# Performance work log

Hardware: AMD Instinct MI355X
Metric: run time of the kernel (lower is better)

Reference implementation:

```python
import jax, jax.numpy as jnp
import numpy as np

B, S, D, H = 2, 2048, 1024, 16
DK = D // H


def setup_inputs() -> dict:
    key = jax.random.key(0)
    ks = jax.random.split(key, 11)
    std = 1.0 / np.sqrt(D)
    return {
        "q": jax.random.normal(ks[0], (B, S, D), jnp.float32),
        "k": jax.random.normal(ks[1], (B, S, D), jnp.float32),
        "v": jax.random.normal(ks[2], (B, S, D), jnp.float32),
        "wq": jax.random.uniform(ks[3], (D, D), jnp.float32, -std, std),
        "bq": jax.random.uniform(ks[4], (D,), jnp.float32, -std, std),
        "wk": jax.random.uniform(ks[5], (D, D), jnp.float32, -std, std),
        "bk": jax.random.uniform(ks[6], (D,), jnp.float32, -std, std),
        "wv": jax.random.uniform(ks[7], (D, D), jnp.float32, -std, std),
        "bv": jax.random.uniform(ks[8], (D,), jnp.float32, -std, std),
        "wo": jax.random.uniform(ks[9], (D, D), jnp.float32, -std, std),
        "bo": jax.random.uniform(ks[10], (D,), jnp.float32, -std, std),
    }


def reference(q, k, v, wq, bq, wk, bk, wv, bv, wo, bo):
    b = q.shape[0]
    # QKV projections (nn.Linear: x @ W.T + b), split into heads -> [b, h, s, dk]
    def proj(x, w, bias):
        y = x @ w.T + bias
        return y.reshape(b, -1, H, DK).transpose(0, 2, 1, 3)

    qh, kh, vh = proj(q, wq, bq), proj(k, wk, bk), proj(v, wv, bv)
    scale = 1.0 / jnp.sqrt(jnp.float32(DK))
    scores = jnp.einsum("bhqd,bhkd->bhqk", qh, kh) * scale  # [b,h,s,s]
    attn = jax.nn.softmax(scores, axis=-1)
    out = jnp.einsum("bhqk,bhkd->bhqd", attn, vh)
    out = out.transpose(0, 2, 1, 3).reshape(b, -1, D)
    out = out @ wo.T + bo
    return out, attn
```

## Files before the change

kernel.cpp:

```cpp
#include <hip/hip_runtime.h>
#include <stdint.h>

#define H 16
#define SEQ 2048
#define DMODEL 1024
#define DK 64

typedef __attribute__((ext_vector_type(8))) short bf16x8;
typedef __attribute__((ext_vector_type(4))) float f32x4;
typedef __attribute__((ext_vector_type(4))) short s16x4;

__device__ __forceinline__ short f2bf(float f) {
  unsigned u = __float_as_uint(f);
  u += 0x7fffu + ((u >> 16) & 1u);
  return (short)(u >> 16);
}

__device__ __forceinline__ f32x4 mfma16(bf16x8 a, bf16x8 b, f32x4 c) {
  return __builtin_amdgcn_mfma_f32_16x16x32_bf16(a, b, c, 0, 0, 0);
}

__global__ void cast_bf16_kernel(const float* __restrict__ src,
                                 short* __restrict__ dst, int n4) {
  int i = blockIdx.x * blockDim.x + threadIdx.x;
  if (i < n4) {
    const float4 v = ((const float4*)src)[i];
    s16x4 o;
    o[0] = f2bf(v.x); o[1] = f2bf(v.y); o[2] = f2bf(v.z); o[3] = f2bf(v.w);
    ((s16x4*)dst)[i] = o;
  }
}

template <int EPI>
__global__ __launch_bounds__(256, 2) void gemm_nt(const short* __restrict__ A,
                                                  const short* __restrict__ Bm,
                                                  const float* __restrict__ bias,
                                                  void* __restrict__ outp) {
  __shared__ short Asub[128 * 32];
  __shared__ short Bsub[128 * 32];
  const int tid = threadIdx.x;
  const int lane = tid & 63, wid = tid >> 6;
  const int g = lane >> 4, ln = lane & 15;
  const int wr = wid >> 1, wc = wid & 1;
  const int m0 = blockIdx.y * 128, n0 = blockIdx.x * 128;

  f32x4 acc[4][4] = {};
  const int f0 = tid, f1 = tid + 256;

  for (int kt = 0; kt < 32; ++kt) {
    const int k0 = kt * 32;
    bf16x8 a0 = *(const bf16x8*)(A + (size_t)(m0 + (f0 >> 2)) * 1024 + k0 + (f0 & 3) * 8);
    bf16x8 a1 = *(const bf16x8*)(A + (size_t)(m0 + (f1 >> 2)) * 1024 + k0 + (f1 & 3) * 8);
    bf16x8 b0 = *(const bf16x8*)(Bm + (size_t)(n0 + (f0 >> 2)) * 1024 + k0 + (f0 & 3) * 8);
    bf16x8 b1 = *(const bf16x8*)(Bm + (size_t)(n0 + (f1 >> 2)) * 1024 + k0 + (f1 & 3) * 8);
    __syncthreads();
    *(bf16x8*)(Asub + f0 * 8) = a0;
    *(bf16x8*)(Asub + f1 * 8) = a1;
    *(bf16x8*)(Bsub + f0 * 8) = b0;
    *(bf16x8*)(Bsub + f1 * 8) = b1;
    __syncthreads();
    bf16x8 af[4], bfr[4];
#pragma unroll
    for (int mi = 0; mi < 4; ++mi)
      af[mi] = *(const bf16x8*)(Asub + (wr * 64 + mi * 16 + ln) * 32 + 8 * g);
#pragma unroll
    for (int ni = 0; ni < 4; ++ni)
      bfr[ni] = *(const bf16x8*)(Bsub + (wc * 64 + ni * 16 + ln) * 32 + 8 * g);
#pragma unroll
    for (int mi = 0; mi < 4; ++mi)
#pragma unroll
      for (int ni = 0; ni < 4; ++ni)
        acc[mi][ni] = mfma16(af[mi], bfr[ni], acc[mi][ni]);
  }

#pragma unroll
  for (int mi = 0; mi < 4; ++mi) {
#pragma unroll
    for (int r = 0; r < 4; ++r) {
      const int row = m0 + wr * 64 + mi * 16 + 4 * g + r;
#pragma unroll
      for (int ni = 0; ni < 4; ++ni) {
        const int col = n0 + wc * 64 + ni * 16 + ln;
        float vv = acc[mi][ni][r];
        if (EPI == 0) {
          vv += bias[col];
          short* dst = (short*)outp;
          const int bb = row >> 11, s = row & 2047, hh = col >> 6, dk = col & 63;
          dst[(size_t)(bb * H + hh) * SEQ * DK + (size_t)s * DK + dk] = f2bf(vv);
        } else if (EPI == 1) {
          vv += bias[row];
          short* dst = (short*)outp;
          const int hh = row >> 6, dk = row & 63, bb = col >> 11, s = col & 2047;
          dst[(size_t)((bb * H + hh) * DK + dk) * SEQ + s] = f2bf(vv);
        } else {
          vv += bias[col];
          ((float*)outp)[(size_t)row * DMODEL + col] = vv;
        }
      }
    }
  }
}

__global__ __launch_bounds__(512, 2) void attn_fused(const short* __restrict__ qh,
                                                     const short* __restrict__ kh,
                                                     const short* __restrict__ vhT,
                                                     float* __restrict__ attn,
                                                     short* __restrict__ oh) {
  __shared__ short p_scr[8][32][40];
  __shared__ float red_max[32][8];
  __shared__ float red_sum[32][8];
  __shared__ float out_red[8][32][68];

  const int tid = threadIdx.x;
  const int w = tid >> 6, lane = tid & 63, g = lane >> 4, ln = lane & 15;
  const int qt = blockIdx.x, hh = blockIdx.y, b = blockIdx.z, bh = b * H + hh;
  const short* Q = qh + (size_t)bh * SEQ * DK;
  const short* K = kh + (size_t)bh * SEQ * DK;
  const short* VT = vhT + (size_t)bh * DK * SEQ;
  float* attn_b = attn + (size_t)bh * SEQ * SEQ;
  const int q0 = qt * 32, jw = w * 256;

  bf16x8 aq[2][2];
#pragma unroll
  for (int mi = 0; mi < 2; ++mi)
#pragma unroll
    for (int kk = 0; kk < 2; ++kk)
      aq[mi][kk] = *(const bf16x8*)(Q + (size_t)(q0 + mi * 16 + ln) * DK + kk * 32 + 8 * g);

  f32x4 acc[2][16] = {};
#pragma unroll
  for (int jt = 0; jt < 16; ++jt) {
    bf16x8 bk0 = *(const bf16x8*)(K + (size_t)(jw + jt * 16 + ln) * DK + 8 * g);
    bf16x8 bk1 = *(const bf16x8*)(K + (size_t)(jw + jt * 16 + ln) * DK + 32 + 8 * g);
#pragma unroll
    for (int mi = 0; mi < 2; ++mi) {
      acc[mi][jt] = mfma16(aq[mi][0], bk0, acc[mi][jt]);
      acc[mi][jt] = mfma16(aq[mi][1], bk1, acc[mi][jt]);
    }
  }

  const float sc = 0.125f;
  float M[2][4], L[2][4];
#pragma unroll
  for (int mi = 0; mi < 2; ++mi)
#pragma unroll
    for (int r = 0; r < 4; ++r) {
      float m = acc[mi][0][r];
#pragma unroll
      for (int jt = 1; jt < 16; ++jt) m = fmaxf(m, acc[mi][jt][r]);
#pragma unroll
      for (int msk = 1; msk <= 8; msk <<= 1) m = fmaxf(m, __shfl_xor(m, msk));
      M[mi][r] = m;
    }
  if (ln == 0) {
#pragma unroll
    for (int mi = 0; mi < 2; ++mi)
#pragma unroll
      for (int r = 0; r < 4; ++r) red_max[mi * 16 + 4 * g + r][w] = M[mi][r];
  }
  __syncthreads();
#pragma unroll
  for (int mi = 0; mi < 2; ++mi)
#pragma unroll
    for (int r = 0; r < 4; ++r) {
      float m = red_max[mi * 16 + 4 * g + r][0];
#pragma unroll
      for (int ww = 1; ww < 8; ++ww) m = fmaxf(m, red_max[mi * 16 + 4 * g + r][ww]);
      M[mi][r] = m;
    }
#pragma unroll
  for (int mi = 0; mi < 2; ++mi)
#pragma unroll
    for (int r = 0; r < 4; ++r) {
      float ssum = 0.f;
#pragma unroll
      for (int jt = 0; jt < 16; ++jt) {
        float p = __expf((acc[mi][jt][r] - M[mi][r]) * sc);
        acc[mi][jt][r] = p;
        ssum += p;
      }
#pragma unroll
      for (int msk = 1; msk <= 8; msk <<= 1) ssum += __shfl_xor(ssum, msk);
      L[mi][r] = ssum;
    }
  if (ln == 0) {
#pragma unroll
    for (int mi = 0; mi < 2; ++mi)
#pragma unroll
      for (int r = 0; r < 4; ++r) red_sum[mi * 16 + 4 * g + r][w] = L[mi][r];
  }
  __syncthreads();
  float inv[2][4];
#pragma unroll
  for (int mi = 0; mi < 2; ++mi)
#pragma unroll
    for (int r = 0; r < 4; ++r) {
      float ssum = red_sum[mi * 16 + 4 * g + r][0];
#pragma unroll
      for (int ww = 1; ww < 8; ++ww) ssum += red_sum[mi * 16 + 4 * g + r][ww];
      inv[mi][r] = 1.0f / ssum;
    }

  f32x4 opv[2][4] = {};
#pragma unroll
  for (int jt2 = 0; jt2 < 8; ++jt2) {
#pragma unroll
    for (int half = 0; half < 2; ++half) {
      const int jt = jt2 * 2 + half;
#pragma unroll
      for (int mi = 0; mi < 2; ++mi)
#pragma unroll
        for (int r = 0; r < 4; ++r) {
          const float p = acc[mi][jt][r] * inv[mi][r];
          const int qrow = mi * 16 + 4 * g + r;
          attn_b[(size_t)(q0 + qrow) * SEQ + jw + jt * 16 + ln] = p;
          p_scr[w][qrow][half * 16 + ln] = f2bf(p);
        }
    }
    __asm__ volatile("s_waitcnt lgkmcnt(0)" ::: "memory");
    __builtin_amdgcn_sched_barrier(0);
    bf16x8 pa[2];
#pragma unroll
    for (int mi = 0; mi < 2; ++mi)
      pa[mi] = *(const bf16x8*)(&p_scr[w][mi * 16 + ln][8 * g]);
#pragma unroll
    for (int di = 0; di < 4; ++di) {
      bf16x8 bv = *(const bf16x8*)(VT + (size_t)(di * 16 + ln) * SEQ + jw + jt2 * 32 + 8 * g);
#pragma unroll
      for (int mi = 0; mi < 2; ++mi) opv[mi][di] = mfma16(pa[mi], bv, opv[mi][di]);
    }
  }

#pragma unroll
  for (int mi = 0; mi < 2; ++mi)
#pragma unroll
    for (int di = 0; di < 4; ++di)
#pragma unroll
      for (int r = 0; r < 4; ++r)
        out_red[w][mi * 16 + 4 * g + r][di * 16 + ln] = opv[mi][di][r];
  __syncthreads();
  const int e0 = tid * 4, qq = e0 >> 6, dd = e0 & 63;
  s16x4 ov;
#pragma unroll
  for (int e = 0; e < 4; ++e) {
    float s = 0.f;
#pragma unroll
    for (int ww = 0; ww < 8; ++ww) s += out_red[ww][qq][dd + e];
    ov[e] = f2bf(s);
  }
  *(s16x4*)(oh + (size_t)(b * SEQ + q0 + qq) * DMODEL + hh * DK + dd) = ov;
}

extern "C" void kernel_launch(void* const* d_in, const int* in_sizes, int n_in,
                              void* d_out, int out_size, void* d_ws, size_t ws_size,
                              hipStream_t stream) {
  (void)in_sizes; (void)n_in; (void)out_size; (void)ws_size;
  const float* q  = (const float*)d_in[0];
  const float* k  = (const float*)d_in[1];
  const float* v  = (const float*)d_in[2];
  const float* wq = (const float*)d_in[3];
  const float* bq = (const float*)d_in[4];
  const float* wk = (const float*)d_in[5];
  const float* bk = (const float*)d_in[6];
  const float* wv = (const float*)d_in[7];
  const float* bv = (const float*)d_in[8];
  const float* wo = (const float*)d_in[9];
  const float* bo = (const float*)d_in[10];

  const size_t NTOK = (size_t)4096 * 1024;
  const size_t NW = (size_t)1024 * 1024;
  short* ws = (short*)d_ws;
  short* xq  = ws;
  short* xk  = xq + NTOK;
  short* xv  = xk + NTOK;
  short* wqb = xv + NTOK;
  short* wkb = wqb + NW;
  short* wvb = wkb + NW;
  short* wob = wvb + NW;
  short* qhb = wob + NW;
  short* khb = qhb + NTOK;
  short* vtb = khb + NTOK;
  short* ohb = vtb + NTOK;

  float* outp  = (float*)d_out;
  float* attnp = outp + NTOK;

  cast_bf16_kernel<<<4096, 256, 0, stream>>>(q, xq, (int)(NTOK / 4));
  cast_bf16_kernel<<<4096, 256, 0, stream>>>(k, xk, (int)(NTOK / 4));
  cast_bf16_kernel<<<4096, 256, 0, stream>>>(v, xv, (int)(NTOK / 4));
  cast_bf16_kernel<<<1024, 256, 0, stream>>>(wq, wqb, (int)(NW / 4));
  cast_bf16_kernel<<<1024, 256, 0, stream>>>(wk, wkb, (int)(NW / 4));
  cast_bf16_kernel<<<1024, 256, 0, stream>>>(wv, wvb, (int)(NW / 4));
  cast_bf16_kernel<<<1024, 256, 0, stream>>>(wo, wob, (int)(NW / 4));

  gemm_nt<0><<<dim3(8, 32), 256, 0, stream>>>(xq, wqb, bq, qhb);
  gemm_nt<0><<<dim3(8, 32), 256, 0, stream>>>(xk, wkb, bk, khb);
  gemm_nt<1><<<dim3(32, 8), 256, 0, stream>>>(wvb, xv, bv, vtb);

  attn_fused<<<dim3(SEQ / 32, H, 2), 512, 0, stream>>>(qhb, khb, vtb, attnp, ohb);

  gemm_nt<2><<<dim3(8, 32), 256, 0, stream>>>(ohb, wob, bo, outp);
}
```

Measured before the change: 872.8 us.

## Fuse cast and QK launches, recompute scores in attention, use direct-to-LDS loads

Merges the seven cast launches into one kernel and the Q and K projection GEMMs into one launch. Switches GEMM tile staging to global_load_lds so data goes straight to shared memory. The attention kernel no longer holds all score accumulators in registers; it recomputes QK^T in three passes (max, sum, final) with exp2. This lowers register pressure so occupancy can rise (launch bounds 4), and the kernel also aliases LDS, swizzles the block order and uses nontemporal stores for the attention matrix. The cost is triple the QK MFMA work and repeated K loads.

Measured after the change: 844.2 us. -3.3%, faster.

```diff
diff --git a/kernel.cpp b/kernel.cpp
--- a/kernel.cpp
+++ b/kernel.cpp
@@ -20,44 +20,66 @@
   return __builtin_amdgcn_mfma_f32_16x16x32_bf16(a, b, c, 0, 0, 0);
 }
 
-__global__ void cast_bf16_kernel(const float* __restrict__ src,
-                                 short* __restrict__ dst, int n4) {
-  int i = blockIdx.x * blockDim.x + threadIdx.x;
-  if (i < n4) {
-    const float4 v = ((const float4*)src)[i];
-    s16x4 o;
-    o[0] = f2bf(v.x); o[1] = f2bf(v.y); o[2] = f2bf(v.z); o[3] = f2bf(v.w);
-    ((s16x4*)dst)[i] = o;
-  }
+__device__ __forceinline__ void gload16(short* lds, const short* g) {
+  __builtin_amdgcn_global_load_lds(
+      (const __attribute__((address_space(1))) unsigned int*)g,
+      (__attribute__((address_space(3))) unsigned int*)lds, 16, 0, 0);
+}
+
+__global__ void cast_all(const float* __restrict__ q, const float* __restrict__ k,
+                         const float* __restrict__ v, const float* __restrict__ wq,
+                         const float* __restrict__ wk, const float* __restrict__ wv,
+                         const float* __restrict__ wo, short* __restrict__ xq,
+                         short* __restrict__ xk, short* __restrict__ xv,
+                         short* __restrict__ wqb, short* __restrict__ wkb,
+                         short* __restrict__ wvb, short* __restrict__ wob) {
+  const int bid = blockIdx.x;
+  const float* src;
+  short* dst;
+  int base;
+  if (bid < 4096) { src = q; dst = xq; base = bid; }
+  else if (bid < 8192) { src = k; dst = xk; base = bid - 4096; }
+  else if (bid < 12288) { src = v; dst = xv; base = bid - 8192; }
+  else if (bid < 13312) { src = wq; dst = wqb; base = bid - 12288; }
+  else if (bid < 14336) { src = wk; dst = wkb; base = bid - 13312; }
+  else if (bid < 15360) { src = wv; dst = wvb; base = bid - 14336; }
+  else { src = wo; dst = wob; base = bid - 15360; }
+  const int i = base * 256 + threadIdx.x;
+  const float4 val = ((const float4*)src)[i];
+  s16x4 o;
+  o[0] = f2bf(val.x); o[1] = f2bf(val.y); o[2] = f2bf(val.z); o[3] = f2bf(val.w);
+  ((s16x4*)dst)[i] = o;
 }
 
 template <int EPI>
-__global__ __launch_bounds__(256, 2) void gemm_nt(const short* __restrict__ A,
-                                                  const short* __restrict__ Bm,
-                                                  const float* __restrict__ bias,
-                                                  void* __restrict__ outp) {
+__device__ __forceinline__ void gemm_body(const short* __restrict__ A,
+                                          const short* __restrict__ Bm,
+                                          const float* __restrict__ bias,
+                                          void* __restrict__ outp,
+                                          const int m0, const int n0) {
   __shared__ short Asub[128 * 32];
   __shared__ short Bsub[128 * 32];
   const int tid = threadIdx.x;
   const int lane = tid & 63, wid = tid >> 6;
   const int g = lane >> 4, ln = lane & 15;
   const int wr = wid >> 1, wc = wid & 1;
-  const int m0 = blockIdx.y * 128, n0 = blockIdx.x * 128;
 
   f32x4 acc[4][4] = {};
   const int f0 = tid, f1 = tid + 256;
+  const int r0 = f0 >> 2, c0 = (f0 & 3) * 8;
+  const int r1 = f1 >> 2, c1 = (f1 & 3) * 8;
+  short* lb0a = Asub + (wid * 64) * 8;
+  short* lb1a = Asub + (256 + wid * 64) * 8;
+  short* lb0b = Bsub + (wid * 64) * 8;
+  short* lb1b = Bsub + (256 + wid * 64) * 8;
 
   for (int kt = 0; kt < 32; ++kt) {
     const int k0 = kt * 32;
-    bf16x8 a0 = *(const bf16x8*)(A + (size_t)(m0 + (f0 >> 2)) * 1024 + k0 + (f0 & 3) * 8);
-    bf16x8 a1 = *(const bf16x8*)(A + (size_t)(m0 + (f1 >> 2)) * 1024 + k0 + (f1 & 3) * 8);
-    bf16x8 b0 = *(const bf16x8*)(Bm + (size_t)(n0 + (f0 >> 2)) * 1024 + k0 + (f0 & 3) * 8);
-    bf16x8 b1 = *(const bf16x8*)(Bm + (size_t)(n0 + (f1 >> 2)) * 1024 + k0 + (f1 & 3) * 8);
     __syncthreads();
-    *(bf16x8*)(Asub + f0 * 8) = a0;
-    *(bf16x8*)(Asub + f1 * 8) = a1;
-    *(bf16x8*)(Bsub + f0 * 8) = b0;
-    *(bf16x8*)(Bsub + f1 * 8) = b1;
+    gload16(lb0a, A + (size_t)(m0 + r0) * 1024 + k0 + c0);
+    gload16(lb1a, A + (size_t)(m0 + r1) * 1024 + k0 + c1);
+    gload16(lb0b, Bm + (size_t)(n0 + r0) * 1024 + k0 + c0);
+    gload16(lb1b, Bm + (size_t)(n0 + r1) * 1024 + k0 + c1);
     __syncthreads();
     bf16x8 af[4], bfr[4];
 #pragma unroll
@@ -101,24 +123,52 @@
   }
 }
 
-__global__ __launch_bounds__(512, 2) void attn_fused(const short* __restrict__ qh,
+__global__ __launch_bounds__(256, 2) void gemm_qk(const short* __restrict__ xq,
+                                                  const short* __restrict__ xk,
+                                                  const short* __restrict__ wqb,
+                                                  const short* __restrict__ wkb,
+                                                  const float* __restrict__ bq,
+                                                  const float* __restrict__ bk,
+                                                  short* __restrict__ qhb,
+                                                  short* __restrict__ khb) {
+  const int seg = blockIdx.x >> 3;
+  const int n0 = (blockIdx.x & 7) * 128;
+  const int m0 = blockIdx.y * 128;
+  gemm_body<0>(seg ? xk : xq, seg ? wkb : wqb, seg ? bk : bq,
+               seg ? (void*)khb : (void*)qhb, m0, n0);
+}
+
+template <int EPI>
+__global__ __launch_bounds__(256, 2) void gemm_nt(const short* __restrict__ A,
+                                                  const short* __restrict__ Bm,
+                                                  const float* __restrict__ bias,
+                                                  void* __restrict__ outp) {
+  gemm_body<EPI>(A, Bm, bias, outp, blockIdx.y * 128, blockIdx.x * 128);
+}
+
+__global__ __launch_bounds__(512, 4) void attn_fused(const short* __restrict__ qh,
                                                      const short* __restrict__ kh,
                                                      const short* __restrict__ vhT,
                                                      float* __restrict__ attn,
                                                      short* __restrict__ oh) {
-  __shared__ short p_scr[8][32][40];
-  __shared__ float red_max[32][8];
-  __shared__ float red_sum[32][8];
-  __shared__ float out_red[8][32][68];
+  __shared__ __align__(16) char smem[8 * 32 * 68 * 4];
+  __shared__ float red_mx[32][8];
+  __shared__ float red_sm[32][8];
+  short (*p_scr)[32][40] = (short (*)[32][40])smem;
+  float (*out_red)[32][68] = (float (*)[32][68])smem;
 
   const int tid = threadIdx.x;
   const int w = tid >> 6, lane = tid & 63, g = lane >> 4, ln = lane & 15;
-  const int qt = blockIdx.x, hh = blockIdx.y, b = blockIdx.z, bh = b * H + hh;
+  int wg = (int)blockIdx.x;
+  wg = (wg & 7) * 256 + (wg >> 3);
+  const int qt = wg & 63, hh = (wg >> 6) & 15, b = wg >> 10;
+  const int bh = b * H + hh;
   const short* Q = qh + (size_t)bh * SEQ * DK;
   const short* K = kh + (size_t)bh * SEQ * DK;
   const short* VT = vhT + (size_t)bh * DK * SEQ;
   float* attn_b = attn + (size_t)bh * SEQ * SEQ;
   const int q0 = qt * 32, jw = w * 256;
+  const float c = 0.18033688f;
 
   bf16x8 aq[2][2];
 #pragma unroll
@@ -127,67 +177,75 @@
     for (int kk = 0; kk < 2; ++kk)
       aq[mi][kk] = *(const bf16x8*)(Q + (size_t)(q0 + mi * 16 + ln) * DK + kk * 32 + 8 * g);
 
-  f32x4 acc[2][16] = {};
-#pragma unroll
+  float mx[2][4];
+#pragma unroll
+  for (int mi = 0; mi < 2; ++mi)
+#pragma unroll
+    for (int r = 0; r < 4; ++r) mx[mi][r] = -3.0e38f;
   for (int jt = 0; jt < 16; ++jt) {
     bf16x8 bk0 = *(const bf16x8*)(K + (size_t)(jw + jt * 16 + ln) * DK + 8 * g);
     bf16x8 bk1 = *(const bf16x8*)(K + (size_t)(jw + jt * 16 + ln) * DK + 32 + 8 * g);
-#pragma unroll
-    for (int mi = 0; mi < 2; ++mi) {
-      acc[mi][jt] = mfma16(aq[mi][0], bk0, acc[mi][jt]);
-      acc[mi][jt] = mfma16(aq[mi][1], bk1, acc[mi][jt]);
-    }
-  }
-
-  const float sc = 0.125f;
-  float M[2][4], L[2][4];
-#pragma unroll
-  for (int mi = 0; mi < 2; ++mi)
-#pragma unroll
-    for (int r = 0; r < 4; ++r) {
-      float m = acc[mi][0][r];
-#pragma unroll
-      for (int jt = 1; jt < 16; ++jt) m = fmaxf(m, acc[mi][jt][r]);
-#pragma unroll
-      for (int msk = 1; msk <= 8; msk <<= 1) m = fmaxf(m, __shfl_xor(m, msk));
+    f32x4 a0 = {}, a1 = {};
+    a0 = mfma16(aq[0][0], bk0, a0);
+    a0 = mfma16(aq[0][1], bk1, a0);
+    a1 = mfma16(aq[1][0], bk0, a1);
+    a1 = mfma16(aq[1][1], bk1, a1);
+#pragma unroll
+    for (int r = 0; r < 4; ++r) {
+      mx[0][r] = fmaxf(mx[0][r], a0[r]);
+      mx[1][r] = fmaxf(mx[1][r], a1[r]);
+    }
+  }
+#pragma unroll
+  for (int msk = 1; msk <= 8; msk <<= 1)
+#pragma unroll
+    for (int mi = 0; mi < 2; ++mi)
+#pragma unroll
+      for (int r = 0; r < 4; ++r) mx[mi][r] = fmaxf(mx[mi][r], __shfl_xor(mx[mi][r], msk));
+  if (ln == 0) {
+#pragma unroll
+    for (int mi = 0; mi < 2; ++mi)
+#pragma unroll
+      for (int r = 0; r < 4; ++r) red_mx[mi * 16 + 4 * g + r][w] = mx[mi][r];
+  }
+  __syncthreads();
+  float M[2][4];
+#pragma unroll
+  for (int mi = 0; mi < 2; ++mi)
+#pragma unroll
+    for (int r = 0; r < 4; ++r) {
+      float m = red_mx[mi * 16 + 4 * g + r][0];
+#pragma unroll
+      for (int ww = 1; ww < 8; ++ww) m = fmaxf(m, red_mx[mi * 16 + 4 * g + r][ww]);
       M[mi][r] = m;
     }
+
+  float sm[2][4] = {};
+  for (int jt = 0; jt < 16; ++jt) {
+    bf16x8 bk0 = *(const bf16x8*)(K + (size_t)(jw + jt * 16 + ln) * DK + 8 * g);
+    bf16x8 bk1 = *(const bf16x8*)(K + (size_t)(jw + jt * 16 + ln) * DK + 32 + 8 * g);
+    f32x4 a0 = {}, a1 = {};
+    a0 = mfma16(aq[0][0], bk0, a0);
+    a0 = mfma16(aq[0][1], bk1, a0);
+    a1 = mfma16(aq[1][0], bk0, a1);
+    a1 = mfma16(aq[1][1], bk1, a1);
+#pragma unroll
+    for (int r = 0; r < 4; ++r) {
+      sm[0][r] += exp2f((a0[r] - M[0][r]) * c);
+      sm[1][r] += exp2f((a1[r] - M[1][r]) * c);
+    }
+  }
+#pragma unroll
+  for (int msk = 1; msk <= 8; msk <<= 1)
+#pragma unroll
+    for (int mi = 0; mi < 2; ++mi)
+#pragma unroll
+      for (int r = 0; r < 4; ++r) sm[mi][r] += __shfl_xor(sm[mi][r], msk);
   if (ln == 0) {
 #pragma unroll
     for (int mi = 0; mi < 2; ++mi)
 #pragma unroll
-      for (int r = 0; r < 4; ++r) red_max[mi * 16 + 4 * g + r][w] = M[mi][r];
-  }
-  __syncthreads();
-#pragma unroll
-  for (int mi = 0; mi < 2; ++mi)
-#pragma unroll
-    for (int r = 0; r < 4; ++r) {
-      float m = red_max[mi * 16 + 4 * g + r][0];
-#pragma unroll
-      for (int ww = 1; ww < 8; ++ww) m = fmaxf(m, red_max[mi * 16 + 4 * g + r][ww]);
-      M[mi][r] = m;
-    }
-#pragma unroll
-  for (int mi = 0; mi < 2; ++mi)
-#pragma unroll
-    for (int r = 0; r < 4; ++r) {
-      float ssum = 0.f;
-#pragma unroll
-      for (int jt = 0; jt < 16; ++jt) {
-        float p = __expf((acc[mi][jt][r] - M[mi][r]) * sc);
-        acc[mi][jt][r] = p;
-        ssum += p;
-      }
-#pragma unroll
-      for (int msk = 1; msk <= 8; msk <<= 1) ssum += __shfl_xor(ssum, msk);
-      L[mi][r] = ssum;
-    }
-  if (ln == 0) {
-#pragma unroll
-    for (int mi = 0; mi < 2; ++mi)
-#pragma unroll
-      for (int r = 0; r < 4; ++r) red_sum[mi * 16 + 4 * g + r][w] = L[mi][r];
+      for (int r = 0; r < 4; ++r) red_sm[mi * 16 + 4 * g + r][w] = sm[mi][r];
   }
   __syncthreads();
   float inv[2][4];
@@ -195,25 +253,32 @@
   for (int mi = 0; mi < 2; ++mi)
 #pragma unroll
     for (int r = 0; r < 4; ++r) {
-      float ssum = red_sum[mi * 16 + 4 * g + r][0];
-#pragma unroll
-      for (int ww = 1; ww < 8; ++ww) ssum += red_sum[mi * 16 + 4 * g + r][ww];
-      inv[mi][r] = 1.0f / ssum;
+      float s = red_sm[mi * 16 + 4 * g + r][0];
+#pragma unroll
+      for (int ww = 1; ww < 8; ++ww) s += red_sm[mi * 16 + 4 * g + r][ww];
+      inv[mi][r] = 1.0f / s;
     }
 
   f32x4 opv[2][4] = {};
-#pragma unroll
   for (int jt2 = 0; jt2 < 8; ++jt2) {
 #pragma unroll
     for (int half = 0; half < 2; ++half) {
       const int jt = jt2 * 2 + half;
+      bf16x8 bk0 = *(const bf16x8*)(K + (size_t)(jw + jt * 16 + ln) * DK + 8 * g);
+      bf16x8 bk1 = *(const bf16x8*)(K + (size_t)(jw + jt * 16 + ln) * DK + 32 + 8 * g);
+      f32x4 a0 = {}, a1 = {};
+      a0 = mfma16(aq[0][0], bk0, a0);
+      a0 = mfma16(aq[0][1], bk1, a0);
+      a1 = mfma16(aq[1][0], bk0, a1);
+      a1 = mfma16(aq[1][1], bk1, a1);
 #pragma unroll
       for (int mi = 0; mi < 2; ++mi)
 #pragma unroll
         for (int r = 0; r < 4; ++r) {
-          const float p = acc[mi][jt][r] * inv[mi][r];
+          const float v = (mi == 0) ? a0[r] : a1[r];
+          const float p = exp2f((v - M[mi][r]) * c) * inv[mi][r];
           const int qrow = mi * 16 + 4 * g + r;
-          attn_b[(size_t)(q0 + qrow) * SEQ + jw + jt * 16 + ln] = p;
+          __builtin_nontemporal_store(p, &attn_b[(size_t)(q0 + qrow) * SEQ + jw + jt * 16 + ln]);
           p_scr[w][qrow][half * 16 + ln] = f2bf(p);
         }
     }
@@ -226,11 +291,12 @@
 #pragma unroll
     for (int di = 0; di < 4; ++di) {
       bf16x8 bv = *(const bf16x8*)(VT + (size_t)(di * 16 + ln) * SEQ + jw + jt2 * 32 + 8 * g);
-#pragma unroll
-      for (int mi = 0; mi < 2; ++mi) opv[mi][di] = mfma16(pa[mi], bv, opv[mi][di]);
-    }
-  }
-
+      opv[0][di] = mfma16(pa[0], bv, opv[0][di]);
+      opv[1][di] = mfma16(pa[1], bv, opv[1][di]);
+    }
+  }
+
+  __syncthreads();
 #pragma unroll
   for (int mi = 0; mi < 2; ++mi)
 #pragma unroll
@@ -285,19 +351,13 @@
   float* outp  = (float*)d_out;
   float* attnp = outp + NTOK;
 
-  cast_bf16_kernel<<<4096, 256, 0, stream>>>(q, xq, (int)(NTOK / 4));
-  cast_bf16_kernel<<<4096, 256, 0, stream>>>(k, xk, (int)(NTOK / 4));
-  cast_bf16_kernel<<<4096, 256, 0, stream>>>(v, xv, (int)(NTOK / 4));
-  cast_bf16_kernel<<<1024, 256, 0, stream>>>(wq, wqb, (int)(NW / 4));
-  cast_bf16_kernel<<<1024, 256, 0, stream>>>(wk, wkb, (int)(NW / 4));
-  cast_bf16_kernel<<<1024, 256, 0, stream>>>(wv, wvb, (int)(NW / 4));
-  cast_bf16_kernel<<<1024, 256, 0, stream>>>(wo, wob, (int)(NW / 4));
-
-  gemm_nt<0><<<dim3(8, 32), 256, 0, stream>>>(xq, wqb, bq, qhb);
-  gemm_nt<0><<<dim3(8, 32), 256, 0, stream>>>(xk, wkb, bk, khb);
+  cast_all<<<16384, 256, 0, stream>>>(q, k, v, wq, wk, wv, wo,
+                                      xq, xk, xv, wqb, wkb, wvb, wob);
+
+  gemm_qk<<<dim3(16, 32), 256, 0, stream>>>(xq, xk, wqb, wkb, bq, bk, qhb, khb);
   gemm_nt<1><<<dim3(32, 8), 256, 0, stream>>>(wvb, xv, bv, vtb);
 
-  attn_fused<<<dim3(SEQ / 32, H, 2), 512, 0, stream>>>(qhb, khb, vtb, attnp, ohb);
+  attn_fused<<<2048, 512, 0, stream>>>(qhb, khb, vtb, attnp, ohb);
 
   gemm_nt<2><<<dim3(8, 32), 256, 0, stream>>>(ohb, wob, bo, outp);
 }
```
